# Kernel optimization log

Measured on AMD Instinct MI355X. Metric: run time of the kernel, lower is better.

The kernel has to match this reference:

```python
import jax, jax.numpy as jnp
import numpy as np
from jax import lax

EPS = 1e-3  # BatchNorm4d eps


def conv4d(x, w, b):
    """4D conv (VALID, stride 1) via kt-shifted 3D convolutions.
    x: [B, Cin, T, D, H, W]; w: [Cout, Cin, kt, kd, kh, kw]; b: [Cout].
    Returns [B, Cout, T', D', H', W']."""
    B, C, T = x.shape[0], x.shape[1], x.shape[2]
    kt = w.shape[2]
    T_out = T - kt + 1
    acc = 0.0
    for i in range(kt):  # tiny fixed loop over kernel's first spatial dim
        xs = x[:, :, i:i + T_out]                              # [B,C,T_out,D,H,W]
        xs = jnp.transpose(xs, (0, 2, 1, 3, 4, 5))             # [B,T_out,C,D,H,W]
        xs = xs.reshape(B * T_out, C, *x.shape[3:])            # fold T_out into batch
        y = lax.conv_general_dilated(
            xs, w[:, :, i], window_strides=(1, 1, 1), padding='VALID',
            dimension_numbers=('NCDHW', 'OIDHW', 'NCDHW'))
        acc = acc + y                                          # [B*T_out,Cout,D',H',W']
    O = w.shape[0]
    y = acc.reshape(B, T_out, O, *acc.shape[2:])
    y = jnp.transpose(y, (0, 2, 1, 3, 4, 5))                   # [B,Cout,T',D',H',W']
    return y + b[None, :, None, None, None, None]


def setup_inputs() -> dict:
    key = jax.random.key(0)
    k = jax.random.split(key, 7)
    Cin, filters, ks = 4, 3, 3
    Cmid, Cout = Cin * filters, Cin * filters * filters        # 12, 36
    x = jax.random.normal(k[0], (8, Cin, 20, 24, 24, 24), dtype=jnp.float32)
    W1 = jax.random.normal(k[1], (Cmid, Cin, ks, ks, ks, ks), dtype=jnp.float32) * 0.05
    b1 = jax.random.normal(k[2], (Cmid,), dtype=jnp.float32) * 0.05
    gamma = jnp.ones((Cmid,), dtype=jnp.float32)
    beta = jnp.zeros((Cmid,), dtype=jnp.float32)
    W2 = jax.random.normal(k[3], (Cout, Cmid, ks, ks, ks, ks), dtype=jnp.float32) * 0.05
    b2 = jax.random.normal(k[4], (Cout,), dtype=jnp.float32) * 0.05
    return {"x": x, "W1": W1, "b1": b1, "gamma": gamma, "beta": beta,
            "W2": W2, "b2": b2}


def reference(x, W1, b1, gamma, beta, W2, b2):
    h = jax.nn.relu(conv4d(x, W1, b1))                         # conv1 -> ReLU
    # BatchNorm4d (training mode: batch statistics over B and all 4 spatial dims)
    mean = jnp.mean(h, axis=(0, 2, 3, 4, 5), keepdims=True)
    var = jnp.var(h, axis=(0, 2, 3, 4, 5), keepdims=True)
    g = gamma[None, :, None, None, None, None]
    bb = beta[None, :, None, None, None, None]
    h = (h - mean) * jax.lax.rsqrt(var + EPS) * g + bb
    h = jax.nn.relu(conv4d(h, W2, b2))                         # conv2 -> ReLU
    return h.reshape(h.shape[0], -1)                           # flatten
```

## Files before the change

### kernel.cpp

```cpp
#include <hip/hip_runtime.h>

#define EPS 0.001f

typedef __attribute__((ext_vector_type(8))) short bf16x8;
typedef __attribute__((ext_vector_type(4))) short bf16x4;
typedef __attribute__((ext_vector_type(4))) float f32x4;

constexpr int Bn = 8, Tx = 20, Dx = 24, Hx = 24, Wx = 24;
constexpr int Cmid = 12, CoutN = 36;
constexpr int T1 = 18, D1 = 22;
constexpr int T2 = 16, D2 = 20;

constexpr int SXD = 576, SXT = 13824, SXC = 276480;
constexpr long SXB = 1105920;

constexpr int XTD = 2304, XTT = 55296;
constexpr long XTB = (long)Tx * XTT;

constexpr int HTW = 16;
constexpr int HTH = 22 * 16;
constexpr int HTD = 22 * 22 * 16;
constexpr int HTT = 22 * HTD;
constexpr long HTB = (long)T1 * HTT;

constexpr int S2D = 400, S2T = 8000, S2O = 128000;
constexpr long S2B = 4608000;

constexpr int NBLK1 = 8 * 18 * 22;

__device__ __forceinline__ unsigned short f2bf(float f) {
    unsigned u = __builtin_bit_cast(unsigned, f);
    u = (u + 0x7fffu + ((u >> 16) & 1u)) >> 16;
    return (unsigned short)u;
}

__device__ __forceinline__ void gload16(const void* g, void* l) {
    __builtin_amdgcn_global_load_lds(
        (const __attribute__((address_space(1))) void*)g,
        (__attribute__((address_space(3))) void*)l, 16, 0, 0);
}

__global__ __launch_bounds__(576) void k_xt(const float* __restrict__ x,
                                            unsigned short* __restrict__ xt) {
    const int tid = threadIdx.x;
    const int d = blockIdx.x, t = blockIdx.y, b = blockIdx.z;
    const float* src = x + (long)b * SXB + (long)t * SXT + (long)d * SXD + tid;
    float v0 = src[0];
    float v1 = src[SXC];
    float v2 = src[2 * SXC];
    float v3 = src[3 * SXC];
    uint2 p;
    p.x = (unsigned)f2bf(v0) | ((unsigned)f2bf(v1) << 16);
    p.y = (unsigned)f2bf(v2) | ((unsigned)f2bf(v3) << 16);
    *(uint2*)(xt + (long)b * XTB + (long)t * XTT + (long)d * XTD + tid * 4) = p;
}

__global__ void k_finW1(const float* __restrict__ W1, unsigned short* __restrict__ Wf1) {
    const int p = blockIdx.x;
    const int lane = threadIdx.x;
    const int m = lane & 15;
    const int q = lane >> 4;
    unsigned short vals[8];
#pragma unroll
    for (int j = 0; j < 8; ++j) {
        int kk = q * 8 + j;
        int g = 2 * p + (kk >> 4);
        int r = kk & 15;
        int kw = r >> 2, cin = r & 3;
        float v = 0.f;
        if (m < 12 && kw < 3 && g < 27) {
            int kt = g / 9, g9 = g - kt * 9, kd = g9 / 3, kh = g9 - kd * 3;
            v = W1[m * 324 + cin * 81 + kt * 27 + kd * 9 + kh * 3 + kw];
        }
        vals[j] = f2bf(v);
    }
    uint4 pk;
    pk.x = (unsigned)vals[0] | ((unsigned)vals[1] << 16);
    pk.y = (unsigned)vals[2] | ((unsigned)vals[3] << 16);
    pk.z = (unsigned)vals[4] | ((unsigned)vals[5] << 16);
    pk.w = (unsigned)vals[6] | ((unsigned)vals[7] << 16);
    *(uint4*)(Wf1 + p * 512 + lane * 8) = pk;
}

__global__ __launch_bounds__(512, 4) void k_conv1m(
    const unsigned short* __restrict__ xt, const unsigned short* __restrict__ Wf1,
    const float* __restrict__ b1, unsigned short* __restrict__ h1t,
    float* __restrict__ part)
{
    __shared__ char lds[9 * 4608 + 16];
    __shared__ float ssum[8][12], ssq[8][12];

    const int tid  = threadIdx.x;
    const int lane = tid & 63;
    const int wv   = tid >> 6;

    const int l  = blockIdx.x;
    const int sw = (l & 7) * 396 + (l >> 3);
    const int d  = sw % 22;
    const int tt = sw / 22;
    const int t  = tt % 18;
    const int b  = tt / 18;
    const int bid = (b * 18 + t) * 22 + d;

    const int n16 = lane & 15;
    const int q   = lane >> 4;

    {
        for (int i = tid; i < 2592; i += 512) {
            int p = i / 288, r = i - p * 288;
            int kt = p / 3, kd = p - kt * 3;
            const unsigned short* src = xt + (long)b * XTB + (long)(t + kt) * XTT
                                      + (long)(d + kd) * XTD + r * 8;
            *(uint4*)(lds + i * 16) = *(const uint4*)src;
        }
    }

    bf16x8 A[14];
#pragma unroll
    for (int p = 0; p < 14; ++p)
        A[p] = *(const bf16x8*)(Wf1 + p * 512 + lane * 8);

    int hh[4], ww[4], nn[4];
#pragma unroll
    for (int u = 0; u < 4; ++u) {
        int n = (wv * 4 + u) * 16 + n16;
        nn[u] = n;
        int nc = n < 484 ? n : 483;
        hh[u] = nc / 22;
        ww[u] = nc - hh[u] * 22;
    }

    f32x4 acc[4];
#pragma unroll
    for (int u = 0; u < 4; ++u) acc[u] = (f32x4){0.f, 0.f, 0.f, 0.f};

    __syncthreads();

#pragma unroll
    for (int p = 0; p < 14; ++p) {
        int gq = 2 * p + (q >> 1);
        int gc = gq < 27 ? gq : 26;
        int kt = gc / 9, g9 = gc - kt * 9, kd = g9 / 3, kh = g9 - kd * 3;
        const int off = (kt * 3 + kd) * 4608 + kh * 192 + (q & 1) * 16;
#pragma unroll
        for (int u = 0; u < 4; ++u) {
            const int addr = off + hh[u] * 192 + ww[u] * 8;
            bf16x4 lo = *(const bf16x4*)(lds + addr);
            bf16x4 hi = *(const bf16x4*)(lds + addr + 8);
            bf16x8 bb;
            bb[0] = lo[0]; bb[1] = lo[1]; bb[2] = lo[2]; bb[3] = lo[3];
            bb[4] = hi[0]; bb[5] = hi[1]; bb[6] = hi[2]; bb[7] = hi[3];
            acc[u] = __builtin_amdgcn_mfma_f32_16x16x32_bf16(A[p], bb, acc[u], 0, 0, 0);
        }
    }

    const int c0 = q * 4;
    float bias[4];
#pragma unroll
    for (int r = 0; r < 4; ++r) bias[r] = (c0 + r) < 12 ? b1[c0 + r] : 0.f;

    float ls[4] = {0.f, 0.f, 0.f, 0.f}, lq[4] = {0.f, 0.f, 0.f, 0.f};
#pragma unroll
    for (int u = 0; u < 4; ++u) {
        const bool valid = nn[u] < 484;
        float v[4];
#pragma unroll
        for (int r = 0; r < 4; ++r) {
            float val = fmaxf(acc[u][r] + bias[r], 0.f);
            v[r] = val;
            if (valid) { ls[r] += val; lq[r] += val * val; }
        }
        if (valid) {
            const long ob = (long)b * HTB + (long)t * HTT + (long)d * HTD
                          + (long)hh[u] * HTH + (long)ww[u] * HTW + c0;
            uint2 pk;
            pk.x = (unsigned)f2bf(v[0]) | ((unsigned)f2bf(v[1]) << 16);
            pk.y = (unsigned)f2bf(v[2]) | ((unsigned)f2bf(v[3]) << 16);
            *(uint2*)(h1t + ob) = pk;
        }
    }

#pragma unroll
    for (int off = 8; off > 0; off >>= 1) {
#pragma unroll
        for (int r = 0; r < 4; ++r) {
            ls[r] += __shfl_xor(ls[r], off);
            lq[r] += __shfl_xor(lq[r], off);
        }
    }
    if (n16 == 0 && q < 3) {
#pragma unroll
        for (int r = 0; r < 4; ++r) {
            ssum[wv][c0 + r] = ls[r];
            ssq[wv][c0 + r] = lq[r];
        }
    }
    __syncthreads();
    if (tid < 12) {
        float s = 0.f;
#pragma unroll
        for (int i = 0; i < 8; ++i) s += ssum[i][tid];
        part[tid * NBLK1 + bid] = s;
    } else if (tid < 24) {
        float s = 0.f;
#pragma unroll
        for (int i = 0; i < 8; ++i) s += ssq[i][tid - 12];
        part[tid * NBLK1 + bid] = s;
    }
}

__global__ void k_red(const float* __restrict__ part, float* __restrict__ stats2) {
    __shared__ float s[256];
    const int c = blockIdx.x;
    const int tid = threadIdx.x;
    float acc = 0.f;
    for (int i = tid; i < NBLK1; i += 256) acc += part[c * NBLK1 + i];
    s[tid] = acc;
    __syncthreads();
    for (int off = 128; off > 0; off >>= 1) {
        if (tid < off) s[tid] += s[tid + off];
        __syncthreads();
    }
    if (tid == 0) stats2[c] = s[0];
}

__global__ void k_fin1(const float* __restrict__ stats2, const float* __restrict__ gamma,
                       const float* __restrict__ beta, const float* __restrict__ W2,
                       const float* __restrict__ b2, float* __restrict__ abuf,
                       float* __restrict__ b2ws)
{
    __shared__ float d_s[12];
    __shared__ float red[36][12];
    const int tid = threadIdx.x;
    if (tid < 12) {
        const float N = 1533312.f;
        float mean = stats2[tid] / N;
        float var  = stats2[12 + tid] / N - mean * mean;
        float a = gamma[tid] * rsqrtf(var + EPS);
        abuf[tid] = a;
        d_s[tid] = beta[tid] - mean * a;
    }
    __syncthreads();
    if (tid < 432) {
        const int o = tid / 12, c = tid - o * 12;
        const float* p = W2 + o * 972 + c * 81;
        float ts = 0.f;
#pragma unroll
        for (int k = 0; k < 81; ++k) ts += p[k];
        red[o][c] = d_s[c] * ts;
    }
    __syncthreads();
    if (tid < 36) {
        float s = b2[tid];
#pragma unroll
        for (int c = 0; c < 12; ++c) s += red[tid][c];
        b2ws[tid] = s;
    }
}

__global__ void k_fin2(const float* __restrict__ W2, const float* __restrict__ abuf,
                       unsigned short* __restrict__ Wf)
{
    const int bi = blockIdx.x;
    const int lane = threadIdx.x;
    const int ch = bi & 1;
    const int tmp = bi >> 1;
    const int mt = tmp % 3;
    const int g = tmp / 3;
    const int kt = g / 9, g9 = g % 9, kd = g9 / 3, kh = g9 % 3;
    const int o = mt * 16 + (lane & 15);

    unsigned short vals[8];
#pragma unroll
    for (int j = 0; j < 8; ++j) {
        int k = ch * 32 + ((lane >> 4) << 3) + j;
        float v = 0.f;
        if (k < 48 && o < 36) {
            int kw = k >> 4, c = k & 15;
            if (c < 12)
                v = W2[o * 972 + c * 81 + kt * 27 + kd * 9 + kh * 3 + kw] * abuf[c];
        }
        vals[j] = f2bf(v);
    }
    uint4 pk;
    pk.x = (unsigned)vals[0] | ((unsigned)vals[1] << 16);
    pk.y = (unsigned)vals[2] | ((unsigned)vals[3] << 16);
    pk.z = (unsigned)vals[4] | ((unsigned)vals[5] << 16);
    pk.w = (unsigned)vals[6] | ((unsigned)vals[7] << 16);
    *(uint4*)(Wf + bi * 512 + lane * 8) = pk;
}

__global__ __launch_bounds__(320, 3) void k_conv2m(
    const unsigned short* __restrict__ h1t, const unsigned short* __restrict__ Wf,
    const float* __restrict__ b2ws, float* __restrict__ out)
{
    __shared__ char lds[2944 * 16];

    const int tid  = threadIdx.x;
    const int lane = tid & 63;
    const int wv   = tid >> 6;

    const int l  = blockIdx.x;
    const int sw = (l & 7) * 320 + (l >> 3);
    const int d  = sw % 20;
    const int tq = sw / 20;
    const int t  = tq & 15;
    const int b  = tq >> 4;

    const int n16 = lane & 15;
    const int q   = lane >> 4;

    int posb[5], pb[5];
#pragma unroll
    for (int u = 0; u < 5; ++u) {
        int p = (wv * 5 + u) * 16 + n16;
        int h = p / 20, w = p - h * 20;
        pb[u] = p;
        posb[u] = h * 704 + w * 32;
    }
    const int qb0 = q * 16;
    const int qb1 = (q & 1) * 16 + 64;

    f32x4 acc[5][3];
#pragma unroll
    for (int u = 0; u < 5; ++u)
#pragma unroll
        for (int mt = 0; mt < 3; ++mt)
            acc[u][mt] = (f32x4){0.f, 0.f, 0.f, 0.f};

    bf16x8 A0[3][2];
#pragma unroll
    for (int mt = 0; mt < 3; ++mt)
#pragma unroll
        for (int c2 = 0; c2 < 2; ++c2)
            A0[mt][c2] = *(const bf16x8*)(Wf + ((mt * 2 + c2) << 9) + lane * 8);

    for (int kt = 0; kt < 3; ++kt) {
        __syncthreads();
        {
            const unsigned short* src = h1t + (long)b * HTB + (long)(t + kt) * HTT
                                      + (long)d * HTD;
#pragma unroll
            for (int r = 0; r < 9; ++r) {
                const int u0 = r * 320 + wv * 64;
                gload16(src + (long)(u0 + lane) * 8, lds + u0 * 16);
            }
            if (wv == 0)
                gload16(src + (long)(2880 + lane) * 8, lds + 2880 * 16);
        }
        __syncthreads();

        for (int g9 = 0; g9 < 9; ++g9) {
            const int g  = kt * 9 + g9;
            const int gn = (g < 26) ? g + 1 : 26;
            const int kd = g9 / 3, kh = g9 - kd * 3;
            const int goff = kd * 15488 + kh * 704;

            bf16x8 A1[3][2];
#pragma unroll
            for (int mt = 0; mt < 3; ++mt)
#pragma unroll
                for (int c2 = 0; c2 < 2; ++c2)
                    A1[mt][c2] = *(const bf16x8*)(Wf + (((gn * 3 + mt) * 2 + c2) << 9) + lane * 8);

#pragma unroll
            for (int u = 0; u < 5; ++u) {
                const char* bbase = lds + posb[u] + goff;
                bf16x8 b0 = *(const bf16x8*)(bbase + qb0);
                bf16x8 b1 = *(const bf16x8*)(bbase + qb1);
#pragma unroll
                for (int mt = 0; mt < 3; ++mt) {
                    acc[u][mt] = __builtin_amdgcn_mfma_f32_16x16x32_bf16(A0[mt][0], b0, acc[u][mt], 0, 0, 0);
                    acc[u][mt] = __builtin_amdgcn_mfma_f32_16x16x32_bf16(A0[mt][1], b1, acc[u][mt], 0, 0, 0);
                }
            }
#pragma unroll
            for (int mt = 0; mt < 3; ++mt)
#pragma unroll
                for (int c2 = 0; c2 < 2; ++c2)
                    A0[mt][c2] = A1[mt][c2];
        }
    }

    const long ob = (long)b * S2B + (long)t * S2T + (long)d * S2D;
#pragma unroll
    for (int mt = 0; mt < 3; ++mt)
#pragma unroll
    for (int r = 0; r < 4; ++r) {
        const int o = mt * 16 + q * 4 + r;
        if (o < 36) {
            const float bias = b2ws[o];
#pragma unroll
            for (int u = 0; u < 5; ++u)
                out[ob + (long)o * S2O + pb[u]] = fmaxf(acc[u][mt][r] + bias, 0.f);
        }
    }
}

extern "C" void kernel_launch(void* const* d_in, const int* in_sizes, int n_in,
                              void* d_out, int out_size, void* d_ws, size_t ws_size,
                              hipStream_t stream) {
    const float* x     = (const float*)d_in[0];
    const float* W1    = (const float*)d_in[1];
    const float* b1    = (const float*)d_in[2];
    const float* gamma = (const float*)d_in[3];
    const float* beta  = (const float*)d_in[4];
    const float* W2    = (const float*)d_in[5];
    const float* b2    = (const float*)d_in[6];
    float* out = (float*)d_out;

    float* ws     = (float*)d_ws;
    float* stats2 = ws;
    float* abuf   = ws + 32;
    float* b2ws   = ws + 64;
    unsigned short* Wf1 = (unsigned short*)((char*)d_ws + 1024);
    unsigned short* Wf  = (unsigned short*)((char*)d_ws + 16384);
    float* part   = (float*)((char*)d_ws + 196608);
    unsigned short* h1t = (unsigned short*)((char*)d_ws + 524288);
    unsigned short* xt  = (unsigned short*)((char*)d_ws + 50331648);

    k_xt<<<dim3(24, 20, 8), 576, 0, stream>>>(x, xt);
    k_finW1<<<14, 64, 0, stream>>>(W1, Wf1);
    k_conv1m<<<3168, 512, 0, stream>>>(xt, Wf1, b1, h1t, part);
    k_red<<<24, 256, 0, stream>>>(part, stats2);
    k_fin1<<<1, 512, 0, stream>>>(stats2, gamma, beta, W2, b2, abuf, b2ws);
    k_fin2<<<162, 64, 0, stream>>>(W2, abuf, Wf);
    k_conv2m<<<2560, 320, 0, stream>>>(h1t, Wf, b2ws, out);
}
```

Measured before the change: 450.4 us.

## Compute two output time steps per conv2 block with double-buffered async slab and weight staging

conv2 blocks now produce two adjacent output t slices, so each loaded input slab (4 slabs for 2 outputs instead of 3 per output) is reused across both. Input slabs and weight fragments are double-buffered in LDS via async global-to-LDS loads, with vmcnt waits and barriers, and the LDS reads use an XOR swizzle to avoid bank conflicts. The conv1 staging also moves from register copies to direct global-to-LDS loads. In exchange the block uses more LDS and accumulators, runs half as many blocks, and depends on a hand-tuned wait schedule.

```diff
diff --git a/kernel.cpp b/kernel.cpp
--- a/kernel.cpp
+++ b/kernel.cpp
@@ -28,6 +28,11 @@
 
 constexpr int NBLK1 = 8 * 18 * 22;
 
+constexpr int SLAB_B_SZ = 49152;
+constexpr int ABUF_OFF  = 2 * SLAB_B_SZ;
+constexpr int ABUF_SZ   = 12288;
+constexpr int LDS_TOT   = ABUF_OFF + 2 * ABUF_SZ;
+
 __device__ __forceinline__ unsigned short f2bf(float f) {
     unsigned u = __builtin_bit_cast(unsigned, f);
     u = (u + 0x7fffu + ((u >> 16) & 1u)) >> 16;
@@ -38,6 +43,10 @@
     __builtin_amdgcn_global_load_lds(
         (const __attribute__((address_space(1))) void*)g,
         (__attribute__((address_space(3))) void*)l, 16, 0, 0);
+}
+
+template<int N> __device__ __forceinline__ void waitvm() {
+    asm volatile("s_waitcnt vmcnt(%0)" :: "i"(N) : "memory");
 }
 
 __global__ __launch_bounds__(576) void k_xt(const float* __restrict__ x,
@@ -106,12 +115,22 @@
     const int q   = lane >> 4;
 
     {
-        for (int i = tid; i < 2592; i += 512) {
-            int p = i / 288, r = i - p * 288;
+#pragma unroll
+        for (int r = 0; r < 5; ++r) {
+            int i = r * 512 + tid;
+            int p = i / 288, rr = i - p * 288;
             int kt = p / 3, kd = p - kt * 3;
             const unsigned short* src = xt + (long)b * XTB + (long)(t + kt) * XTT
-                                      + (long)(d + kd) * XTD + r * 8;
-            *(uint4*)(lds + i * 16) = *(const uint4*)src;
+                                      + (long)(d + kd) * XTD + rr * 8;
+            gload16(src, lds + (r * 512 + wv * 64) * 16);
+        }
+        if (tid < 32) {
+            int i = 2560 + tid;
+            int p = i / 288, rr = i - p * 288;
+            int kt = p / 3, kd = p - kt * 3;
+            const unsigned short* src = xt + (long)b * XTB + (long)(t + kt) * XTT
+                                      + (long)(d + kd) * XTD + rr * 8;
+            gload16(src, lds + 2560 * 16);
         }
     }
 
@@ -290,109 +309,168 @@
     *(uint4*)(Wf + bi * 512 + lane * 8) = pk;
 }
 
-__global__ __launch_bounds__(320, 3) void k_conv2m(
+__global__ __launch_bounds__(512, 2) void k_conv2m(
     const unsigned short* __restrict__ h1t, const unsigned short* __restrict__ Wf,
     const float* __restrict__ b2ws, float* __restrict__ out)
 {
-    __shared__ char lds[2944 * 16];
+    __shared__ char lds[LDS_TOT];
 
     const int tid  = threadIdx.x;
     const int lane = tid & 63;
     const int wv   = tid >> 6;
 
-    const int l  = blockIdx.x;
-    const int sw = (l & 7) * 320 + (l >> 3);
-    const int d  = sw % 20;
-    const int tq = sw / 20;
-    const int t  = tq & 15;
-    const int b  = tq >> 4;
+    const int l   = blockIdx.x;
+    const int b   = l & 7;
+    const int rem = l >> 3;
+    const int d   = rem % 20;
+    const int t0  = (rem / 20) * 2;
 
     const int n16 = lane & 15;
     const int q   = lane >> 4;
 
-    int posb[5], pb[5];
-#pragma unroll
-    for (int u = 0; u < 5; ++u) {
-        int p = (wv * 5 + u) * 16 + n16;
-        int h = p / 20, w = p - h * 20;
-        pb[u] = p;
-        posb[u] = h * 704 + w * 32;
-    }
-    const int qb0 = q * 16;
-    const int qb1 = (q & 1) * 16 + 64;
-
-    f32x4 acc[5][3];
-#pragma unroll
-    for (int u = 0; u < 5; ++u)
-#pragma unroll
-        for (int mt = 0; mt < 3; ++mt)
-            acc[u][mt] = (f32x4){0.f, 0.f, 0.f, 0.f};
-
-    bf16x8 A0[3][2];
-#pragma unroll
-    for (int mt = 0; mt < 3; ++mt)
-#pragma unroll
-        for (int c2 = 0; c2 < 2; ++c2)
-            A0[mt][c2] = *(const bf16x8*)(Wf + ((mt * 2 + c2) << 9) + lane * 8);
-
-    for (int kt = 0; kt < 3; ++kt) {
-        __syncthreads();
-        {
-            const unsigned short* src = h1t + (long)b * HTB + (long)(t + kt) * HTT
-                                      + (long)d * HTD;
-#pragma unroll
-            for (int r = 0; r < 9; ++r) {
-                const int u0 = r * 320 + wv * 64;
-                gload16(src + (long)(u0 + lane) * 8, lds + u0 * 16);
+    auto stage_slab = [&](int ktIn, int buf) {
+        const unsigned short* base = h1t + (long)b * HTB + (long)(t0 + ktIn) * HTT
+                                   + (long)d * HTD;
+#pragma unroll
+        for (int r = 0; r < 6; ++r) {
+            int j = r * 512 + wv * 64 + lane;
+            int f = ((j % 44) >> 3) & 1;
+            gload16(base + (long)(j ^ f) * 8,
+                    lds + buf * SLAB_B_SZ + (r * 512 + wv * 64) * 16);
+        }
+    };
+    auto stage_A = [&](int tt) {
+        const int dstb = ABUF_OFF + (tt & 1) * ABUF_SZ;
+#pragma unroll
+        for (int r = 0; r < 2; ++r) {
+            int j  = wv * 96 + r * 32 + lane;
+            int fi = j >> 6;
+            int sl = j & 63;
+            int pe = fi / 6;
+            int r6 = fi - pe * 6;
+            int mt = r6 >> 1, ch = r6 & 1;
+            int gA = tt - pe * 9;
+            gA = (gA >= 0 && gA < 27) ? gA : 0;
+            int idx = (gA * 3 + mt) * 2 + ch;
+            gload16(Wf + idx * 512 + sl * 8,
+                    lds + dstb + (wv * 96 + r * 32) * 16);
+        }
+    };
+
+    int rb0a[4], rb1a[4], pba[4];
+    bool val[4];
+#pragma unroll
+    for (int ps = 0; ps < 4; ++ps) {
+        int pt = ps * 8 + wv;
+        val[ps] = pt < 25;
+        int ptc = val[ps] ? pt : 0;
+        int n = ptc * 16 + n16;
+        int h = n / 20, w = n - h * 20;
+        pba[ps] = n;
+        int posb = n / 20 * 704 + w * 32;
+        int u0 = 2 * w + q;
+        int u1 = 2 * w + 4 + (q & 1);
+        rb0a[ps] = (posb + q * 16) ^ (((u0 >> 3) & 1) << 4);
+        rb1a[ps] = (posb + (q & 1) * 16 + 64) ^ (((u1 >> 3) & 1) << 4);
+        (void)h;
+    }
+
+    f32x4 acc[4][2][3];
+#pragma unroll
+    for (int ps = 0; ps < 4; ++ps)
+#pragma unroll
+        for (int pe = 0; pe < 2; ++pe)
+#pragma unroll
+            for (int mt = 0; mt < 3; ++mt)
+                acc[ps][pe][mt] = (f32x4){0.f, 0.f, 0.f, 0.f};
+
+    stage_slab(0, 0);
+    stage_A(0);
+
+#define COMPUTE_STEP(KT, G9V, PE0, PE1)                                          \
+  {                                                                              \
+    const int g9_ = (G9V);                                                       \
+    const int kd_ = g9_ / 3, kh_ = g9_ - kd_ * 3;                                \
+    const int goff_ = kd_ * 15488 + kh_ * 704;                                   \
+    const char* sbp_ = lds + ((KT) & 1) * SLAB_B_SZ;                             \
+    const char* abp_ = lds + ABUF_OFF + (((KT) * 9 + g9_) & 1) * ABUF_SZ;        \
+    bf16x8 Af0_[3][2], Af1_[3][2];                                               \
+    if (PE0) {                                                                   \
+      _Pragma("unroll") for (int mt = 0; mt < 3; ++mt)                           \
+        _Pragma("unroll") for (int ch = 0; ch < 2; ++ch)                         \
+          Af0_[mt][ch] = *(const bf16x8*)(abp_ + (mt * 2 + ch) * 1024 + lane * 16); \
+    }                                                                            \
+    if (PE1) {                                                                   \
+      _Pragma("unroll") for (int mt = 0; mt < 3; ++mt)                           \
+        _Pragma("unroll") for (int ch = 0; ch < 2; ++ch)                         \
+          Af1_[mt][ch] = *(const bf16x8*)(abp_ + (6 + mt * 2 + ch) * 1024 + lane * 16); \
+    }                                                                            \
+    __builtin_amdgcn_s_setprio(1);                                               \
+    _Pragma("unroll")                                                            \
+    for (int ps = 0; ps < 4; ++ps) if (val[ps]) {                                \
+      bf16x8 b0_ = *(const bf16x8*)(sbp_ + rb0a[ps] + goff_);                    \
+      bf16x8 b1_ = *(const bf16x8*)(sbp_ + rb1a[ps] + goff_);                    \
+      if (PE0) {                                                                 \
+        _Pragma("unroll") for (int mt = 0; mt < 3; ++mt) {                       \
+          acc[ps][0][mt] = __builtin_amdgcn_mfma_f32_16x16x32_bf16(Af0_[mt][0], b0_, acc[ps][0][mt], 0, 0, 0); \
+          acc[ps][0][mt] = __builtin_amdgcn_mfma_f32_16x16x32_bf16(Af0_[mt][1], b1_, acc[ps][0][mt], 0, 0, 0); \
+        }                                                                        \
+      }                                                                          \
+      if (PE1) {                                                                 \
+        _Pragma("unroll") for (int mt = 0; mt < 3; ++mt) {                       \
+          acc[ps][1][mt] = __builtin_amdgcn_mfma_f32_16x16x32_bf16(Af1_[mt][0], b0_, acc[ps][1][mt], 0, 0, 0); \
+          acc[ps][1][mt] = __builtin_amdgcn_mfma_f32_16x16x32_bf16(Af1_[mt][1], b1_, acc[ps][1][mt], 0, 0, 0); \
+        }                                                                        \
+      }                                                                          \
+    }                                                                            \
+    __builtin_amdgcn_s_setprio(0);                                               \
+  }
+
+#define FULL_STEP(KT, G9V, VMN, DOSLAB)                                          \
+  {                                                                              \
+    const int s_ = (KT) * 9 + (G9V);                                             \
+    if (s_ < 35) stage_A(s_ + 1);                                                \
+    if (DOSLAB) stage_slab((KT) + 1, ((KT) + 1) & 1);                            \
+    waitvm<VMN>();                                                               \
+    __builtin_amdgcn_s_barrier();                                                \
+    __builtin_amdgcn_sched_barrier(0);                                           \
+    COMPUTE_STEP(KT, G9V, ((KT) < 3), ((KT) > 0))                                \
+    __builtin_amdgcn_s_barrier();                                                \
+  }
+
+    for (int g9 = 0; g9 < 4; ++g9) FULL_STEP(0, g9, 2, false)
+    FULL_STEP(0, 4, 8, true)
+    FULL_STEP(0, 5, 8, false)
+    for (int g9 = 6; g9 < 9; ++g9) FULL_STEP(0, g9, 2, false)
+    for (int g9 = 0; g9 < 4; ++g9) FULL_STEP(1, g9, 2, false)
+    FULL_STEP(1, 4, 8, true)
+    FULL_STEP(1, 5, 8, false)
+    for (int g9 = 6; g9 < 9; ++g9) FULL_STEP(1, g9, 2, false)
+    for (int g9 = 0; g9 < 4; ++g9) FULL_STEP(2, g9, 2, false)
+    FULL_STEP(2, 4, 8, true)
+    FULL_STEP(2, 5, 8, false)
+    for (int g9 = 6; g9 < 9; ++g9) FULL_STEP(2, g9, 2, false)
+    for (int g9 = 0; g9 < 8; ++g9) FULL_STEP(3, g9, 2, false)
+    FULL_STEP(3, 8, 0, false)
+
+#undef FULL_STEP
+#undef COMPUTE_STEP
+
+    const long obase = (long)b * S2B + (long)d * S2D;
+#pragma unroll
+    for (int ps = 0; ps < 4; ++ps) if (val[ps]) {
+#pragma unroll
+        for (int pe = 0; pe < 2; ++pe) {
+            const long ot = obase + (long)(t0 + pe) * S2T;
+#pragma unroll
+            for (int mt = 0; mt < 3; ++mt)
+#pragma unroll
+            for (int r = 0; r < 4; ++r) {
+                const int o = mt * 16 + q * 4 + r;
+                if (o < 36)
+                    out[ot + (long)o * S2O + pba[ps]] =
+                        fmaxf(acc[ps][pe][mt][r] + b2ws[o], 0.f);
             }
-            if (wv == 0)
-                gload16(src + (long)(2880 + lane) * 8, lds + 2880 * 16);
-        }
-        __syncthreads();
-
-        for (int g9 = 0; g9 < 9; ++g9) {
-            const int g  = kt * 9 + g9;
-            const int gn = (g < 26) ? g + 1 : 26;
-            const int kd = g9 / 3, kh = g9 - kd * 3;
-            const int goff = kd * 15488 + kh * 704;
-
-            bf16x8 A1[3][2];
-#pragma unroll
-            for (int mt = 0; mt < 3; ++mt)
-#pragma unroll
-                for (int c2 = 0; c2 < 2; ++c2)
-                    A1[mt][c2] = *(const bf16x8*)(Wf + (((gn * 3 + mt) * 2 + c2) << 9) + lane * 8);
-
-#pragma unroll
-            for (int u = 0; u < 5; ++u) {
-                const char* bbase = lds + posb[u] + goff;
-                bf16x8 b0 = *(const bf16x8*)(bbase + qb0);
-                bf16x8 b1 = *(const bf16x8*)(bbase + qb1);
-#pragma unroll
-                for (int mt = 0; mt < 3; ++mt) {
-                    acc[u][mt] = __builtin_amdgcn_mfma_f32_16x16x32_bf16(A0[mt][0], b0, acc[u][mt], 0, 0, 0);
-                    acc[u][mt] = __builtin_amdgcn_mfma_f32_16x16x32_bf16(A0[mt][1], b1, acc[u][mt], 0, 0, 0);
-                }
-            }
-#pragma unroll
-            for (int mt = 0; mt < 3; ++mt)
-#pragma unroll
-                for (int c2 = 0; c2 < 2; ++c2)
-                    A0[mt][c2] = A1[mt][c2];
-        }
-    }
-
-    const long ob = (long)b * S2B + (long)t * S2T + (long)d * S2D;
-#pragma unroll
-    for (int mt = 0; mt < 3; ++mt)
-#pragma unroll
-    for (int r = 0; r < 4; ++r) {
-        const int o = mt * 16 + q * 4 + r;
-        if (o < 36) {
-            const float bias = b2ws[o];
-#pragma unroll
-            for (int u = 0; u < 5; ++u)
-                out[ob + (long)o * S2O + pb[u]] = fmaxf(acc[u][mt][r] + bias, 0.f);
         }
     }
 }
@@ -425,5 +503,5 @@
     k_red<<<24, 256, 0, stream>>>(part, stats2);
     k_fin1<<<1, 512, 0, stream>>>(stats2, gamma, beta, W2, b2, abuf, b2ws);
     k_fin2<<<162, 64, 0, stream>>>(W2, abuf, Wf);
-    k_conv2m<<<2560, 320, 0, stream>>>(h1t, Wf, b2ws, out);
-}
+    k_conv2m<<<1280, 512, 0, stream>>>(h1t, Wf, b2ws, out);
+}
```

Measured after the change: 420.5 us. -6.7%, faster.
